# Kernel optimization log

Measured on AMD Instinct MI355X. Metric: run time of the kernel, lower is better.

## Reference

```python
import jax, jax.numpy as jnp
import numpy as np

N, C, D = 1024, 151, 4096   # num boxes, num classes (VG-150+bg), hidden_dim*8
NMS_THRESH = 0.5            # cfg.TEST.RELATION.LATER_NMS_PREDICTION_THRES


def setup_inputs() -> dict:
    key = jax.random.key(0)
    k1, k2, k3, k4 = jax.random.split(key, 4)
    obj_fmap = jax.random.normal(k1, (N, D), jnp.float32)
    W_out = jax.random.normal(k2, (D, C), jnp.float32) / np.sqrt(D).astype(np.float32)
    b_out = jnp.zeros((C,), jnp.float32)
    # valid xyxy boxes: top-left in [0,800), width/height in [16,208)
    xy = jax.random.uniform(k3, (N, C, 2), jnp.float32, 0.0, 800.0)
    wh = jax.random.uniform(k4, (N, C, 2), jnp.float32, 16.0, 208.0)
    boxes_per_cls = jnp.concatenate([xy, xy + wh], axis=-1)  # [N, C, 4]
    return {"obj_fmap": obj_fmap, "W_out": W_out, "b_out": b_out,
            "boxes_per_cls": boxes_per_cls}


def nms_overlaps(boxes):
    """Per-class pairwise IoU. boxes: [N, C, 4] xyxy -> [N, N, C].
    Matches neural-motifs nms_overlaps (uses the +1 pixel convention)."""
    max_xy = jnp.minimum(boxes[:, None, :, 2:], boxes[None, :, :, 2:])  # [N,N,C,2]
    min_xy = jnp.maximum(boxes[:, None, :, :2], boxes[None, :, :, :2])  # [N,N,C,2]
    inter_wh = jnp.clip(max_xy - min_xy + 1.0, 0.0)
    inters = inter_wh[..., 0] * inter_wh[..., 1]                         # [N,N,C]
    areas = (boxes[..., 2] - boxes[..., 0] + 1.0) * \
            (boxes[..., 3] - boxes[..., 1] + 1.0)                        # [N,C]
    union = areas[None, :, :] + areas[:, None, :] - inters
    return inters / union


def greedy_commit(probs, is_overlap):
    """Greedy per-box class commitment with overlap suppression.
    probs: [N,C] (background col already zeroed); is_overlap: [N,N,C] bool."""
    n, c = probs.shape
    row_ids = jnp.arange(n)
    col_ids = jnp.arange(c)

    def body(i, state):
        p, commits = state
        flat = jnp.argmax(p)
        b, cl = flat // c, flat % c
        commits = jnp.where(row_ids == b, cl, commits)
        ov = is_overlap[b, :, cl]                      # [N] dynamic gather
        # zero column cl for overlapping boxes
        p = jnp.where((col_ids[None, :] == cl) & ov[:, None], 0.0, p)
        # retire the committed box
        p = jnp.where((row_ids == b)[:, None], -1.0, p)
        return p, commits

    _, commits = jax.lax.fori_loop(0, n, body,
                                   (probs, jnp.zeros((n,), jnp.int32)))
    return commits


def reference(obj_fmap, W_out, b_out, boxes_per_cls):
    # decoder: obj_dists2 = self.out_obj(obj_fmap)
    obj_dists = obj_fmap @ W_out + b_out                 # [N, C]
    # sgdet eval branch: softmax scores, zero background, greedy NMS commit
    probs = jax.nn.softmax(obj_dists, axis=-1)
    probs = probs.at[:, 0].set(0.0)
    is_overlap = nms_overlaps(boxes_per_cls) >= NMS_THRESH  # [N,N,C] bool
    obj_preds = greedy_commit(probs, is_overlap)            # [N] int32
    return obj_dists, obj_preds
```

## Files before the change

### kernel.cpp

```cpp
#include <hip/hip_runtime.h>

#define NB 1024
#define NC 151
#define NCP 152
#define DF 4096
typedef unsigned long long u64;

__global__ __launch_bounds__(192) void gemm_sm_kernel(
    const float* __restrict__ fmap, const float* __restrict__ W,
    const float* __restrict__ bias, float* __restrict__ dists,
    float* __restrict__ probs) {
  __shared__ float sf[4 * DF];
  __shared__ float sdist[4][NCP];
  __shared__ float smx[4], ssum[4];
  int r0 = blockIdx.x * 4;
  const float4* src = (const float4*)(fmap + (size_t)r0 * DF);
  for (int i = threadIdx.x; i < 4 * (DF / 4); i += 192) {
    int r = i >> 10;
    int q = i & 1023;
    float4 v = src[i];
    sf[(4 * q + 0) * 4 + r] = v.x;
    sf[(4 * q + 1) * 4 + r] = v.y;
    sf[(4 * q + 2) * 4 + r] = v.z;
    sf[(4 * q + 3) * 4 + r] = v.w;
  }
  __syncthreads();
  int c = threadIdx.x;
  if (c < NC) {
    double a0 = 0.0, a1 = 0.0, a2 = 0.0, a3 = 0.0;
    const float* w = W + c;
    const float4* sf4 = (const float4*)sf;
#pragma unroll 8
    for (int d = 0; d < DF; ++d) {
      float4 f = sf4[d];
      double wv = (double)w[(size_t)d * NC];
      a0 += (double)f.x * wv;
      a1 += (double)f.y * wv;
      a2 += (double)f.z * wv;
      a3 += (double)f.w * wv;
    }
    float b = bias[c];
    float v0 = (float)a0 + b, v1 = (float)a1 + b, v2 = (float)a2 + b, v3 = (float)a3 + b;
    dists[(size_t)(r0 + 0) * NC + c] = v0;
    dists[(size_t)(r0 + 1) * NC + c] = v1;
    dists[(size_t)(r0 + 2) * NC + c] = v2;
    dists[(size_t)(r0 + 3) * NC + c] = v3;
    sdist[0][c] = v0; sdist[1][c] = v1; sdist[2][c] = v2; sdist[3][c] = v3;
  }
  __syncthreads();
  if (threadIdx.x < 64) {
    int t = threadIdx.x;
#pragma unroll
    for (int r = 0; r < 4; ++r) {
      float v0 = sdist[r][t];
      float v1 = sdist[r][t + 64];
      float v2 = (t + 128 < NC) ? sdist[r][t + 128] : -3.0e38f;
      float m = fmaxf(fmaxf(v0, v1), v2);
      for (int off = 32; off; off >>= 1) m = fmaxf(m, __shfl_down(m, off));
      m = __shfl(m, 0);
      float e0 = expf(v0 - m), e1 = expf(v1 - m);
      float e2 = (t + 128 < NC) ? expf(v2 - m) : 0.0f;
      float s = e0 + e1 + e2;
      for (int off = 32; off; off >>= 1) s += __shfl_down(s, off);
      s = __shfl(s, 0);
      if (t == 0) { smx[r] = m; ssum[r] = s; }
    }
  }
  __syncthreads();
  if (c < NC) {
#pragma unroll
    for (int r = 0; r < 4; ++r) {
      float p = (c == 0) ? 0.0f : (expf(sdist[r][c] - smx[r]) / ssum[r]);
      probs[(size_t)(r0 + r) * NCP + c] = p;
    }
  }
  if (threadIdx.x == 0) {
#pragma unroll
    for (int r = 0; r < 4; ++r) probs[(size_t)(r0 + r) * NCP + NC] = -1.0f;
  }
}

__global__ __launch_bounds__(256) void mask_kernel(
    const float* __restrict__ boxes, u64* __restrict__ mask) {
#pragma clang fp contract(off)
  int cl = blockIdx.x >> 4;
  int bb = (blockIdx.x & 15) * 64;
  __shared__ float4 sbox[NB];
  __shared__ float sarea[NB];
  for (int i = threadIdx.x; i < NB; i += 256) {
    float4 b = *(const float4*)(boxes + ((size_t)i * NC + cl) * 4);
    sbox[i] = b;
    sarea[i] = (b.z - b.x + 1.0f) * (b.w - b.y + 1.0f);
  }
  __syncthreads();
  int wv = threadIdx.x >> 6, lane = threadIdx.x & 63;
  for (int j = 0; j < 16; ++j) {
    int b = bb + wv * 16 + j;
    float4 B = sbox[b];
    float areaB = sarea[b];
    u64 myword = 0;
#pragma unroll
    for (int k = 0; k < 16; ++k) {
      int r = k * 64 + lane;
      float4 R = sbox[r];
      float ix = fminf(B.z, R.z) - fmaxf(B.x, R.x) + 1.0f;
      float iy = fminf(B.w, R.w) - fmaxf(B.y, R.y) + 1.0f;
      ix = fmaxf(ix, 0.0f);
      iy = fmaxf(iy, 0.0f);
      float inter = ix * iy;
      float uni = sarea[r] + areaB - inter;
      float iou = inter / uni;
      u64 bal = __ballot(iou >= 0.5f);
      if (lane == k) myword = bal;
    }
    if (lane < 16) mask[((size_t)cl * NB + b) * 16 + lane] = myword;
  }
}

template <int CTRL, int ROWMASK>
__device__ __forceinline__ float dpp_max_step(float v) {
  int x = __float_as_int(v);
  int t = __builtin_amdgcn_update_dpp(x, x, CTRL, ROWMASK, 0xf, false);
  return fmaxf(v, __int_as_float(t));
}

__device__ __forceinline__ float wave_max(float v) {
  v = dpp_max_step<0x111, 0xf>(v);
  v = dpp_max_step<0x112, 0xf>(v);
  v = dpp_max_step<0x114, 0xf>(v);
  v = dpp_max_step<0x118, 0xf>(v);
  v = dpp_max_step<0x142, 0xa>(v);
  v = dpp_max_step<0x143, 0xc>(v);
  return __int_as_float(__builtin_amdgcn_readlane(__float_as_int(v), 63));
}

__device__ __forceinline__ void rescan_row(const float* __restrict__ pp,
                                           u64 z0, u64 z1, u64 z2,
                                           float& mo, int& ao) {
  const float4* p4 = (const float4*)pp;
  float m = 0.0f; int a = 0;
#pragma unroll 2
  for (int q = 0; q < NCP / 4; ++q) {
    float4 v = p4[q];
    u64 z = q < 16 ? z0 : (q < 32 ? z1 : z2);
    unsigned bits = (unsigned)(z >> ((q & 15) * 4)) & 0xFu;
    int c0 = q * 4;
    float vx = (bits & 1u) ? 0.0f : v.x;
    float vy = (bits & 2u) ? 0.0f : v.y;
    float vz = (bits & 4u) ? 0.0f : v.z;
    float vw = (bits & 8u) ? 0.0f : v.w;
    if (vx > m) { m = vx; a = c0; }
    if (vy > m) { m = vy; a = c0 + 1; }
    if (vz > m) { m = vz; a = c0 + 2; }
    if (vw > m) { m = vw; a = c0 + 3; }
  }
  mo = m; ao = a;
}

__global__ __launch_bounds__(256, 1) void greedy_kernel(
    const float* __restrict__ probs, const u64* __restrict__ mask,
    float* __restrict__ out_preds) {
  __shared__ u64 smask[NB * 16];
  __shared__ unsigned pcls[NB];
  __shared__ u64 skey[2][4];

  int tid = threadIdx.x;
  int w = tid >> 6, lane = tid & 63;
  int rbase = tid << 2;
  int widx = tid >> 4;
  int hsh = (tid & 15) << 2;

  float rm[4];
  int ra[4], cm[4];
  u64 zb0[4], zb1[4], zb2[4];
  unsigned committed = 0;

#pragma unroll
  for (int r = 0; r < 4; ++r) {
    rescan_row(probs + (size_t)(rbase + r) * NCP, 0, 0, 0, rm[r], ra[r]);
    cm[r] = 0; zb0[r] = 0; zb1[r] = 0; zb2[r] = 0;
    pcls[rbase + r] = (unsigned)ra[r];
  }
  __syncthreads();

  for (int j = 0; j < NB; j += 16) {
    int col = j + (tid >> 4);
    int wd = tid & 15;
    unsigned pc = pcls[col];
    smask[(col << 4) | wd] = mask[(((size_t)pc << 10) | (size_t)col) * 16 + wd];
  }
  __syncthreads();

  for (int it = 0; it < NB; ++it) {
    int par = it & 1;

    float bv = rm[0];
    int bp = ra[0];
#pragma unroll
    for (int r = 1; r < 4; ++r) {
      int p = (r << 8) | ra[r];
      bool t = rm[r] > bv;
      bv = t ? rm[r] : bv;
      bp = t ? p : bp;
    }

    float wmax = wave_max(bv);
    u64 ball = __ballot(bv == wmax);
    int wl = __ffsll(ball) - 1;
    int pw = __builtin_amdgcn_readlane(bp, wl);
    int gw = (w << 8) | (wl << 2) | (pw >> 8);
    int clw = pw & 0xff;
    unsigned ub = __float_as_uint(wmax);
    unsigned su = ((int)ub >= 0) ? (ub | 0x80000000u) : ~ub;
    u64 key = ((u64)su << 32) | ((u64)(NB - 1 - gw) << 8) | (unsigned)clw;
    if (lane == 0) skey[par][w] = key;
    __syncthreads();

    u64 k0 = skey[par][0], k1 = skey[par][1], k2 = skey[par][2], k3 = skey[par][3];
    u64 ka = k0 > k1 ? k0 : k1;
    u64 kb = k2 > k3 ? k2 : k3;
    u64 kk = ka > kb ? ka : kb;
    int b = NB - 1 - (int)((kk >> 8) & 0x3FFu);
    int cl = (int)(kk & 0xFFu);

    unsigned pc = pcls[b];
    u64 word;
    if ((unsigned)cl == pc) {
      word = smask[(b << 4) | widx];
    } else {
      word = mask[(((size_t)cl << 10) | (size_t)b) * 16 + widx];
    }
    unsigned hits = (unsigned)(word >> hsh) & 0xFu;

    int wi = cl >> 6;
    u64 bmv = 1ull << (cl & 63);
    u64 m0 = (wi == 0) ? bmv : 0, m1 = (wi == 1) ? bmv : 0, m2 = (wi == 2) ? bmv : 0;

    bool meT = (tid == (b >> 2));
    int blo = b & 3;

    unsigned need = 0;
#pragma unroll
    for (int r = 0; r < 4; ++r) {
      unsigned rb = 1u << r;
      bool hit = (hits & rb) != 0;
      if (r == blo) {
        if (meT) { committed |= rb; rm[r] = -1.0f; cm[r] = cl; hit = false; }
      }
      if (hit) {
        if (committed & rb) {
          if (rm[r] < 0.0f) { rm[r] = 0.0f; ra[r] = cl; }
          else if (cl < ra[r]) ra[r] = cl;
        } else {
          zb0[r] |= m0; zb1[r] |= m1; zb2[r] |= m2;
          if (ra[r] == cl) need |= rb;
        }
      }
    }
    if (__ballot(need != 0)) {
#pragma unroll
      for (int r = 0; r < 4; ++r) {
        if (need & (1u << r))
          rescan_row(probs + (size_t)(rbase + r) * NCP,
                     zb0[r], zb1[r], zb2[r], rm[r], ra[r]);
      }
    }
  }

#pragma unroll
  for (int r = 0; r < 4; ++r)
    out_preds[rbase + r] = (float)cm[r];
}

extern "C" void kernel_launch(void* const* d_in, const int* in_sizes, int n_in,
                              void* d_out, int out_size, void* d_ws, size_t ws_size,
                              hipStream_t stream) {
  const float* obj_fmap = (const float*)d_in[0];
  const float* W_out    = (const float*)d_in[1];
  const float* b_out    = (const float*)d_in[2];
  const float* boxes    = (const float*)d_in[3];

  float* out_dists = (float*)d_out;
  float* out_preds = (float*)d_out + NB * NC;

  float* probs = (float*)d_ws;
  u64*   mask  = (u64*)(probs + (size_t)NB * NCP);

  gemm_sm_kernel<<<NB / 4, 192, 0, stream>>>(obj_fmap, W_out, b_out, out_dists, probs);
  mask_kernel<<<NC * 16, 256, 0, stream>>>(boxes, mask);
  greedy_kernel<<<1, 256, 0, stream>>>(probs, mask, out_preds);
}
```

Before: 1.076 ms.

## Commit two greedy picks per round when the second is unaffected by the first

The greedy loop now finds the top two candidates (value, row, class) per wave and across the block in each round. When the second pick has a positive score and is not suppressed by the first (different class, or no overlap bit), both are committed in the same round, halving the number of block-wide barriers and reductions in the best case. This adds a second wave reduction, extra mask lookups and more complex correctness conditions. Whether the second pick stays valid after the first commit's suppression and any rescans is subtle and could change results.

Result: slower. 1.129 ms (+4.9%).

```diff
diff --git a/kernel.cpp b/kernel.cpp
--- a/kernel.cpp
+++ b/kernel.cpp
@@ -162,7 +162,7 @@
     float* __restrict__ out_preds) {
   __shared__ u64 smask[NB * 16];
   __shared__ unsigned pcls[NB];
-  __shared__ u64 skey[2][4];
+  __shared__ u64 skey[2][4][2];
 
   int tid = threadIdx.x;
   int w = tid >> 6, lane = tid & 63;
@@ -191,55 +191,12 @@
   }
   __syncthreads();
 
-  for (int it = 0; it < NB; ++it) {
-    int par = it & 1;
-
-    float bv = rm[0];
-    int bp = ra[0];
-#pragma unroll
-    for (int r = 1; r < 4; ++r) {
-      int p = (r << 8) | ra[r];
-      bool t = rm[r] > bv;
-      bv = t ? rm[r] : bv;
-      bp = t ? p : bp;
-    }
-
-    float wmax = wave_max(bv);
-    u64 ball = __ballot(bv == wmax);
-    int wl = __ffsll(ball) - 1;
-    int pw = __builtin_amdgcn_readlane(bp, wl);
-    int gw = (w << 8) | (wl << 2) | (pw >> 8);
-    int clw = pw & 0xff;
-    unsigned ub = __float_as_uint(wmax);
-    unsigned su = ((int)ub >= 0) ? (ub | 0x80000000u) : ~ub;
-    u64 key = ((u64)su << 32) | ((u64)(NB - 1 - gw) << 8) | (unsigned)clw;
-    if (lane == 0) skey[par][w] = key;
-    __syncthreads();
-
-    u64 k0 = skey[par][0], k1 = skey[par][1], k2 = skey[par][2], k3 = skey[par][3];
-    u64 ka = k0 > k1 ? k0 : k1;
-    u64 kb = k2 > k3 ? k2 : k3;
-    u64 kk = ka > kb ? ka : kb;
-    int b = NB - 1 - (int)((kk >> 8) & 0x3FFu);
-    int cl = (int)(kk & 0xFFu);
-
-    unsigned pc = pcls[b];
-    u64 word;
-    if ((unsigned)cl == pc) {
-      word = smask[(b << 4) | widx];
-    } else {
-      word = mask[(((size_t)cl << 10) | (size_t)b) * 16 + widx];
-    }
-    unsigned hits = (unsigned)(word >> hsh) & 0xFu;
-
+  auto apply = [&](int b, int cl, unsigned hits, unsigned& need) {
     int wi = cl >> 6;
     u64 bmv = 1ull << (cl & 63);
-    u64 m0 = (wi == 0) ? bmv : 0, m1 = (wi == 1) ? bmv : 0, m2 = (wi == 2) ? bmv : 0;
-
+    u64 q0 = (wi == 0) ? bmv : 0, q1 = (wi == 1) ? bmv : 0, q2 = (wi == 2) ? bmv : 0;
     bool meT = (tid == (b >> 2));
     int blo = b & 3;
-
-    unsigned need = 0;
 #pragma unroll
     for (int r = 0; r < 4; ++r) {
       unsigned rb = 1u << r;
@@ -252,11 +209,96 @@
           if (rm[r] < 0.0f) { rm[r] = 0.0f; ra[r] = cl; }
           else if (cl < ra[r]) ra[r] = cl;
         } else {
-          zb0[r] |= m0; zb1[r] |= m1; zb2[r] |= m2;
+          zb0[r] |= q0; zb1[r] |= q1; zb2[r] |= q2;
           if (ra[r] == cl) need |= rb;
         }
       }
     }
+  };
+
+  int done = 0, rnd = 0;
+  while (done < NB) {
+    int par = rnd & 1;
+    ++rnd;
+
+    float m1 = -2.0f, m2 = -2.0f;
+    int a1 = 0, a2 = 0;
+#pragma unroll
+    for (int r = 0; r < 4; ++r) {
+      float v = rm[r];
+      int p = (r << 8) | ra[r];
+      if (v > m1) { m2 = m1; a2 = a1; m1 = v; a1 = p; }
+      else if (v > m2) { m2 = v; a2 = p; }
+    }
+
+    float wm1 = wave_max(m1);
+    u64 ba1 = __ballot(m1 == wm1);
+    int wl1 = __ffsll(ba1) - 1;
+    int pw1 = __builtin_amdgcn_readlane(a1, wl1);
+    float c2 = (lane == wl1) ? m2 : m1;
+    int p2l = (lane == wl1) ? a2 : a1;
+    float wm2 = wave_max(c2);
+    u64 ba2 = __ballot(c2 == wm2);
+    int wl2 = __ffsll(ba2) - 1;
+    int pw2 = __builtin_amdgcn_readlane(p2l, wl2);
+
+    if (lane == 0) {
+      int row1 = (w << 8) | (wl1 << 2) | (pw1 >> 8);
+      unsigned u1 = __float_as_uint(wm1);
+      unsigned s1 = ((int)u1 >= 0) ? (u1 | 0x80000000u) : ~u1;
+      skey[par][w][0] = ((u64)s1 << 32) | ((u64)(NB - 1 - row1) << 8) | (unsigned)(pw1 & 0xff);
+      int row2 = (w << 8) | (wl2 << 2) | (pw2 >> 8);
+      unsigned u2 = __float_as_uint(wm2);
+      unsigned s2 = ((int)u2 >= 0) ? (u2 | 0x80000000u) : ~u2;
+      skey[par][w][1] = ((u64)s2 << 32) | ((u64)(NB - 1 - row2) << 8) | (unsigned)(pw2 & 0xff);
+    }
+    __syncthreads();
+
+    u64 kv[8];
+#pragma unroll
+    for (int i = 0; i < 8; ++i) kv[i] = skey[par][i >> 1][i & 1];
+    u64 kk1 = kv[0];
+#pragma unroll
+    for (int i = 1; i < 8; ++i) kk1 = kv[i] > kk1 ? kv[i] : kk1;
+    u64 kk2 = 0;
+#pragma unroll
+    for (int i = 0; i < 8; ++i) {
+      u64 x = (kv[i] == kk1) ? 0ull : kv[i];
+      kk2 = x > kk2 ? x : kk2;
+    }
+
+    int b1 = NB - 1 - (int)((kk1 >> 8) & 0x3FFu);
+    int cl1 = (int)(kk1 & 0xFFu);
+    int b2 = NB - 1 - (int)((kk2 >> 8) & 0x3FFu);
+    int cl2 = (int)(kk2 & 0xFFu);
+    unsigned su2 = (unsigned)(kk2 >> 32);
+
+    unsigned pc1 = pcls[b1], pc2 = pcls[b2];
+    bool f1 = ((unsigned)cl1 == pc1), f2 = ((unsigned)cl2 == pc2);
+    u64 wordA, wordB, wordChk;
+    if (f1 && f2) {
+      wordA = smask[(b1 << 4) | widx];
+      wordB = smask[(b2 << 4) | widx];
+      wordChk = smask[(b1 << 4) | (b2 >> 6)];
+    } else {
+      wordA = f1 ? smask[(b1 << 4) | widx]
+                 : mask[(((size_t)cl1 << 10) | (size_t)b1) * 16 + widx];
+      wordB = f2 ? smask[(b2 << 4) | widx]
+                 : mask[(((size_t)cl2 << 10) | (size_t)b2) * 16 + widx];
+      wordChk = f1 ? smask[(b1 << 4) | (b2 >> 6)]
+                   : mask[(((size_t)cl1 << 10) | (size_t)b1) * 16 + (b2 >> 6)];
+    }
+    unsigned hitsA = (unsigned)(wordA >> hsh) & 0xFu;
+    unsigned hitsB = (unsigned)(wordB >> hsh) & 0xFu;
+
+    bool bitChk = ((wordChk >> (b2 & 63)) & 1ull) != 0;
+    bool v2 = (su2 > 0x80000000u) && !(bitChk && (cl1 == cl2)) && (done + 2 <= NB);
+
+    unsigned need = 0;
+    apply(b1, cl1, hitsA, need);
+    if (v2) apply(b2, cl2, hitsB, need);
+    done += v2 ? 2 : 1;
+
     if (__ballot(need != 0)) {
 #pragma unroll
       for (int r = 0; r < 4; ++r) {
```
